# Kernel optimization log

Hardware: AMD Instinct MI355X
Metric: run time of the kernel (lower is better)

Reference implementation:

```python
import jax, jax.numpy as jnp
import numpy as np

D_MODEL = 1024
D_INNER = 2048
D_STATE = 16
DT_RANK = 64  # ceil(1024/16)
N_LAYERS = 4
SEQ = 4096


def setup_inputs() -> dict:
    key = jax.random.key(0)
    ks = list(jax.random.split(key, 8))
    L, d, di, n, r = N_LAYERS, D_MODEL, D_INNER, D_STATE, DT_RANK
    def rn(k, shape, scale):
        return jax.random.normal(k, shape, dtype=jnp.float32) * scale
    A_init = jnp.tile(jnp.log(jnp.arange(1, n + 1, dtype=jnp.float32))[None, None, :], (L, di, 1))
    return {
        'x': jax.random.normal(ks[0], (SEQ, d), dtype=jnp.float32),
        'pos_enc': jax.random.normal(ks[1], (SEQ, d), dtype=jnp.float32),
        'ln_g': jnp.ones((d,), jnp.float32),
        'ln_b': jnp.zeros((d,), jnp.float32),
        'innorm_g': jnp.ones((L, d), jnp.float32),
        'innorm_b': jnp.zeros((L, d), jnp.float32),
        'in_proj_w': rn(ks[2], (L, 2 * di, d), 0.02),
        'in_proj_b': jnp.zeros((L, 2 * di), jnp.float32),
        'conv_w': rn(ks[3], (L, di, 1, 3), 0.1),
        'conv_b': jnp.zeros((L, di), jnp.float32),
        'deltaBC_w': rn(ks[4], (L, r + 2 * n, di), 0.02),
        'dt_proj_w': rn(ks[5], (L, di, r), 0.02),
        'dt_proj_b': jnp.zeros((L, di), jnp.float32),
        'A_log': A_init,
        'Dp': jnp.ones((L, di), jnp.float32),
        'outnorm_g': jnp.ones((L, di), jnp.float32),
        'outnorm_b': jnp.zeros((L, di), jnp.float32),
        'out_proj_w': rn(ks[6], (L, d, di), 0.02),
        'out_proj_b': jnp.zeros((L, d), jnp.float32),
    }


def _ln(x, g, b, eps):
    mu = jnp.mean(x, axis=-1, keepdims=True)
    var = jnp.mean((x - mu) ** 2, axis=-1, keepdims=True)
    return (x - mu) * jax.lax.rsqrt(var + eps) * g + b


def _selective_scan(u, delta, A, B, C, D):
    # u, delta: [b,l,d]; A: [d,n]; B, C: [b,l,n]; D: [d]
    b, l, d = u.shape
    n = A.shape[1]
    def step(h, inputs):
        d_t, B_t, u_t, C_t = inputs          # [b,d],[b,n],[b,d],[b,n]
        dA = jnp.exp(d_t[:, :, None] * A)    # [b,d,n]
        dBu = (d_t * u_t)[:, :, None] * B_t[:, None, :]
        h = dA * h + dBu
        y = jnp.einsum('bdn,bn->bd', h, C_t)
        return h, y
    h0 = jnp.zeros((b, d, n), u.dtype)
    xs = (jnp.swapaxes(delta, 0, 1), jnp.swapaxes(B, 0, 1),
          jnp.swapaxes(u, 0, 1), jnp.swapaxes(C, 0, 1))
    _, ys = jax.lax.scan(step, h0, xs)       # ys: [l,b,d]
    return jnp.swapaxes(ys, 0, 1) + u * D


def _block(x, innorm_g, innorm_b, in_proj_w, in_proj_b, conv_w, conv_b,
           deltaBC_w, dt_proj_w, dt_proj_b, A_log, Dp, outnorm_g, outnorm_b,
           out_proj_w, out_proj_b):
    skip = x
    h = _ln(x, innorm_g, innorm_b, 1e-5)
    xz = h @ in_proj_w.T + in_proj_b
    x1, z1 = jnp.split(xz, 2, axis=-1)       # [b,s,di] each
    # depthwise conv1d, k=3, pad=1
    xc = jnp.swapaxes(x1, 1, 2)              # [b,di,s]
    xc = jax.lax.conv_general_dilated(xc, conv_w, (1,), [(1, 1)],
                                      feature_group_count=xc.shape[1],
                                      dimension_numbers=('NCH', 'OIH', 'NCH'))
    xc = xc + conv_b[None, :, None]
    u = jnp.swapaxes(xc, 1, 2)               # [b,s,di]
    # SSM
    A = -jnp.exp(A_log)
    dbc = u @ deltaBC_w.T                    # [b,s,r+2n]
    delta, B, C = jnp.split(dbc, [DT_RANK, DT_RANK + D_STATE], axis=-1)
    delta = jax.nn.softplus(delta @ dt_proj_w.T + dt_proj_b)
    y = _selective_scan(u, delta, A, B, C, Dp)
    y = _ln(y, outnorm_g, outnorm_b, 1e-5)
    out = y * jax.nn.silu(z1)
    return out @ out_proj_w.T + out_proj_b + skip


def _forward(x, pos_enc, ln_g, ln_b, innorm_g, innorm_b, in_proj_w, in_proj_b,
             conv_w, conv_b, deltaBC_w, dt_proj_w, dt_proj_b, A_log, Dp,
             outnorm_g, outnorm_b, out_proj_w, out_proj_b):
    enc = _ln(x + pos_enc, ln_g, ln_b, 1e-6)[None]  # [1,s,d]
    for i in range(N_LAYERS):
        enc = _block(enc, innorm_g[i], innorm_b[i], in_proj_w[i], in_proj_b[i],
                     conv_w[i], conv_b[i], deltaBC_w[i], dt_proj_w[i],
                     dt_proj_b[i], A_log[i], Dp[i], outnorm_g[i], outnorm_b[i],
                     out_proj_w[i], out_proj_b[i])
    return enc[0]


def reference(x, pos_enc, ln_g, ln_b, innorm_g, innorm_b, in_proj_w, in_proj_b,
              conv_w, conv_b, deltaBC_w, dt_proj_w, dt_proj_b, A_log, Dp,
              outnorm_g, outnorm_b, out_proj_w, out_proj_b):
    return _forward(x, pos_enc, ln_g, ln_b, innorm_g, innorm_b, in_proj_w,
                    in_proj_b, conv_w, conv_b, deltaBC_w, dt_proj_w, dt_proj_b,
                    A_log, Dp, outnorm_g, outnorm_b, out_proj_w, out_proj_b)
```

## Files before the change

kernel.cpp:

```cpp
#include <hip/hip_runtime.h>
#include <hip/hip_bf16.h>
#include <stdint.h>


#define SEQ     4096
#define DMODEL  1024
#define DINNER  2048
#define NSTATE  16
#define DTRANK  64
#define NLAYERS 4
#define LC      64
#define NC      64

typedef __attribute__((ext_vector_type(8))) short short8v;
typedef __attribute__((ext_vector_type(4))) float f32x4;
typedef __hip_bfloat16 bf16;

__device__ __forceinline__ float b2f(unsigned short x) {
    unsigned int u = ((unsigned int)x) << 16;
    return __builtin_bit_cast(float, u);
}

__device__ __forceinline__ void gld16(const void* gsrc, void* ldst) {
    __builtin_amdgcn_global_load_lds(
        (const __attribute__((address_space(1))) void*)gsrc,
        (__attribute__((address_space(3))) void*)ldst, 16, 0, 0);
}

__device__ __forceinline__ float block_sum(float v, float* red, int nwaves) {
    #pragma unroll
    for (int o = 32; o > 0; o >>= 1) v += __shfl_down(v, o, 64);
    int lane = threadIdx.x & 63, w = threadIdx.x >> 6;
    __syncthreads();
    if (lane == 0) red[w] = v;
    __syncthreads();
    float s = red[0];
    for (int i = 1; i < nwaves; i++) s += red[i];
    return s;
}

template<int WIDTH, typename OutT>
__global__ void ln_kernel(const float* __restrict__ X, const float* __restrict__ X2,
                          const float* __restrict__ g, const float* __restrict__ bta,
                          OutT* __restrict__ out, float eps) {
    constexpr int E = WIDTH / 256;
    __shared__ float red[4];
    int s = blockIdx.x, tid = threadIdx.x;
    size_t base = (size_t)s * WIDTH;
    float v[E]; float sum = 0.f;
    #pragma unroll
    for (int i = 0; i < E; i++) {
        int c = tid + i * 256;
        float t = X[base + c];
        if (X2) t += X2[base + c];
        v[i] = t; sum += t;
    }
    float mu = block_sum(sum, red, 4) * (1.f / WIDTH);
    float sq = 0.f;
    #pragma unroll
    for (int i = 0; i < E; i++) { float d = v[i] - mu; sq += d * d; }
    float var = block_sum(sq, red, 4) * (1.f / WIDTH);
    float rstd = rsqrtf(var + eps);
    #pragma unroll
    for (int i = 0; i < E; i++) {
        int c = tid + i * 256;
        float r = (v[i] - mu) * rstd * g[c] + bta[c];
        out[base + c] = (OutT)r;
    }
}

__global__ void outnorm_silu_kernel(const float* __restrict__ y, const bf16* __restrict__ xz,
                                    const float* __restrict__ g, const float* __restrict__ bta,
                                    bf16* __restrict__ p_bf, float eps) {
    constexpr int WIDTH = DINNER, E = WIDTH / 256;
    __shared__ float red[4];
    int s = blockIdx.x, tid = threadIdx.x;
    size_t base = (size_t)s * WIDTH;
    const unsigned short* xzu = (const unsigned short*)xz;
    float v[E]; float sum = 0.f;
    #pragma unroll
    for (int i = 0; i < E; i++) { int c = tid + i * 256; v[i] = y[base + c]; sum += v[i]; }
    float mu = block_sum(sum, red, 4) * (1.f / WIDTH);
    float sq = 0.f;
    #pragma unroll
    for (int i = 0; i < E; i++) { float d = v[i] - mu; sq += d * d; }
    float var = block_sum(sq, red, 4) * (1.f / WIDTH);
    float rstd = rsqrtf(var + eps);
    #pragma unroll
    for (int i = 0; i < E; i++) {
        int c = tid + i * 256;
        float ln = (v[i] - mu) * rstd * g[c] + bta[c];
        float z = b2f(xzu[(size_t)s * (2 * DINNER) + DINNER + c]);
        float sig = 1.f / (1.f + __expf(-z));
        p_bf[base + c] = __float2bfloat16(ln * (z * sig));
    }
}

__global__ void conv_kernel(const bf16* __restrict__ xz, const float* __restrict__ cw,
                            const float* __restrict__ cb, bf16* __restrict__ u_bf) {
    int t = blockIdx.x * 256 + threadIdx.x;
    int s = t >> 9, c = (t & 511) * 4;
    size_t row = (size_t)s * (2 * DINNER);
    const unsigned short* xp = (const unsigned short*)xz;
    ushort4 z4 = {0, 0, 0, 0};
    ushort4 v0 = *(const ushort4*)(xp + row + c);
    ushort4 vm = (s > 0)       ? *(const ushort4*)(xp + row - 2 * DINNER + c) : z4;
    ushort4 vp = (s < SEQ - 1) ? *(const ushort4*)(xp + row + 2 * DINNER + c) : z4;
    unsigned short o[4];
    float x0[4] = {b2f(v0.x), b2f(v0.y), b2f(v0.z), b2f(v0.w)};
    float xm[4] = {b2f(vm.x), b2f(vm.y), b2f(vm.z), b2f(vm.w)};
    float xp4[4] = {b2f(vp.x), b2f(vp.y), b2f(vp.z), b2f(vp.w)};
    #pragma unroll
    for (int i = 0; i < 4; i++) {
        int ch = c + i;
        float u = cw[ch * 3 + 0] * xm[i] + cw[ch * 3 + 1] * x0[i]
                + cw[ch * 3 + 2] * xp4[i] + cb[ch];
        o[i] = __builtin_bit_cast(unsigned short, __float2bfloat16(u));
    }
    *(ushort4*)((unsigned short*)u_bf + (size_t)s * DINNER + c) = {o[0], o[1], o[2], o[3]};
}

#define CN0 (2 * DINNER * DMODEL)
#define CN1 (DMODEL * DINNER)
#define CN2 (96 * DINNER)
#define CN3 (DINNER * DTRANK)
__global__ void cvt_all_kernel(const float* __restrict__ w0, const float* __restrict__ w1,
                               const float* __restrict__ w2, const float* __restrict__ w3,
                               bf16* __restrict__ o0, bf16* __restrict__ o1,
                               bf16* __restrict__ o2, bf16* __restrict__ o3) {
    size_t i = (size_t)(blockIdx.x * 256 + threadIdx.x) * 4;
    const float* src; bf16* dst;
    if (i < CN0)                   { src = w0; dst = o0; }
    else if (i < CN0 + CN1)        { src = w1; dst = o1; i -= CN0; }
    else if (i < CN0 + CN1 + CN2)  { src = w2; dst = o2; i -= CN0 + CN1; }
    else                           { src = w3; dst = o3; i -= CN0 + CN1 + CN2; }
    float4 v = *(const float4*)(src + i);
    __hip_bfloat162 t0, t1;
    t0.x = __float2bfloat16(v.x); t0.y = __float2bfloat16(v.y);
    t1.x = __float2bfloat16(v.z); t1.y = __float2bfloat16(v.w);
    __hip_bfloat162* o = (__hip_bfloat162*)(dst + i);
    o[0] = t0; o[1] = t1;
}

template<int MODE>
__global__ __launch_bounds__(256, 2)
void mfma_gemm(const bf16* __restrict__ A, int lda,
               const bf16* __restrict__ W, int ldw,
               const float* __restrict__ bias,
               float* __restrict__ C, int ldc,
               const float* __restrict__ res,
               bf16* __restrict__ Cbf,
               int M, int N, int K) {
    __shared__ __attribute__((aligned(16))) short sA[128][32];
    __shared__ __attribute__((aligned(16))) short sB[128][32];
    int tid = threadIdx.x;
    int lane = tid & 63, w = tid >> 6;
    int wm = w >> 1, wn = w & 1;
    int m0 = blockIdx.x * 128, n0 = blockIdx.y * 128;
    int r16 = lane & 15, quad = lane >> 4;
    int ldrow = (lane >> 2);
    int c8 = (lane & 3) * 8;

    if (MODE == 1) {
        int kz = blockIdx.z;
        A += (size_t)kz * K;
        W += (size_t)kz * K;
        C += (size_t)kz * M * 96;
    }

    f32x4 acc[4][4] = {};

    for (int k0 = 0; k0 < K; k0 += 32) {
        __syncthreads();
        #pragma unroll
        for (int j = 0; j < 2; j++) {
            int row = j * 64 + w * 16 + ldrow;
            gld16(A + (size_t)(m0 + row) * lda + k0 + c8,
                  (char*)&sA[0][0] + j * 4096 + w * 1024);
            int nr = n0 + row; if (nr > N - 1) nr = N - 1;
            gld16(W + (size_t)nr * ldw + k0 + c8,
                  (char*)&sB[0][0] + j * 4096 + w * 1024);
        }
        __syncthreads();
        short8v aF[4], bF[4];
        #pragma unroll
        for (int mi = 0; mi < 4; mi++)
            aF[mi] = *(const short8v*)&sA[wm * 64 + mi * 16 + r16][quad * 8];
        #pragma unroll
        for (int ni = 0; ni < 4; ni++)
            bF[ni] = *(const short8v*)&sB[wn * 64 + ni * 16 + r16][quad * 8];
        #pragma unroll
        for (int mi = 0; mi < 4; mi++)
            #pragma unroll
            for (int ni = 0; ni < 4; ni++)
                acc[mi][ni] = __builtin_amdgcn_mfma_f32_16x16x32_bf16(
                    aF[mi], bF[ni], acc[mi][ni], 0, 0, 0);
    }

    #pragma unroll
    for (int mi = 0; mi < 4; mi++) {
        #pragma unroll
        for (int ni = 0; ni < 4; ni++) {
            f32x4 a = acc[mi][ni];
            int col = n0 + wn * 64 + ni * 16 + r16;
            int rbase = m0 + wm * 64 + mi * 16 + quad * 4;
            #pragma unroll
            for (int r = 0; r < 4; r++) {
                int row = rbase + r;
                float v = a[r];
                if (MODE == 0 || MODE == 2 || MODE == 3) v += bias[col];
                if (MODE == 2) v = (v > 20.f) ? v : log1pf(__expf(v));
                if (MODE == 3) v += res[(size_t)row * ldc + col];
                if (MODE == 1) {
                    if (col < 96) C[(size_t)row * 96 + col] = v;
                } else if (MODE == 0) {
                    Cbf[(size_t)row * ldc + col] = __float2bfloat16(v);
                } else {
                    C[(size_t)row * ldc + col] = v;
                }
            }
        }
    }
}

__global__ void reduce_dbc_kernel(const float* __restrict__ p, float* __restrict__ dbc,
                                  bf16* __restrict__ dbc_bf) {
    int i = blockIdx.x * 256 + threadIdx.x;
    const int SP = SEQ * 96;
    float v = p[i] + p[i + SP] + p[i + 2 * SP] + p[i + 3 * SP];
    dbc[i] = v;
    int row = i / 96, c = i - row * 96;
    if (c < DTRANK) dbc_bf[(size_t)row * DTRANK + c] = __float2bfloat16(v);
}

__device__ __forceinline__ bool a_is_neg_integers(const float* a) {
    bool fast = true;
    #pragma unroll
    for (int n = 0; n < NSTATE; n++)
        fast = fast && (__builtin_fabsf(a[n] + (float)(n + 1)) < 1e-3f * (n + 1));
    return fast;
}

__global__ __launch_bounds__(256)
void scan1_kernel(const float* __restrict__ delta, const bf16* __restrict__ u,
                  const float* __restrict__ dbc, const float* __restrict__ A_log,
                  float* __restrict__ h_end, float* __restrict__ dsum) {
    int k = blockIdx.x, d = blockIdx.y * 256 + threadIdx.x;
    int s0 = k * LC;
    float a[NSTATE];
    #pragma unroll
    for (int n = 0; n < NSTATE; n++) a[n] = -__expf(A_log[(size_t)d * NSTATE + n]);
    bool fast = a_is_neg_integers(a);
    const float* dp = delta + (size_t)s0 * DINNER + d;
    const unsigned short* up = (const unsigned short*)u + (size_t)s0 * DINNER + d;
    const float* br = dbc + (size_t)s0 * 96 + DTRANK;
    float h[NSTATE] = {};
    float ds = 0.f;
    if (fast) {
        #pragma unroll 2
        for (int r = 0; r < LC; r++) {
            float dl = *dp;
            float uu = b2f(*up);
            float4 b0 = *(const float4*)(br);
            float4 b1 = *(const float4*)(br + 4);
            float4 b2 = *(const float4*)(br + 8);
            float4 b3 = *(const float4*)(br + 12);
            float Bv[NSTATE] = {b0.x, b0.y, b0.z, b0.w, b1.x, b1.y, b1.z, b1.w,
                                b2.x, b2.y, b2.z, b2.w, b3.x, b3.y, b3.z, b3.w};
            ds += dl;
            float du = dl * uu;
            float g = __expf(-dl);
            float fac = 1.f;
            #pragma unroll
            for (int n = 0; n < NSTATE; n++) {
                fac *= g;
                h[n] = fac * h[n] + du * Bv[n];
            }
            dp += DINNER; up += DINNER; br += 96;
        }
    } else {
        #pragma unroll 2
        for (int r = 0; r < LC; r++) {
            float dl = *dp;
            float uu = b2f(*up);
            float4 b0 = *(const float4*)(br);
            float4 b1 = *(const float4*)(br + 4);
            float4 b2 = *(const float4*)(br + 8);
            float4 b3 = *(const float4*)(br + 12);
            float Bv[NSTATE] = {b0.x, b0.y, b0.z, b0.w, b1.x, b1.y, b1.z, b1.w,
                                b2.x, b2.y, b2.z, b2.w, b3.x, b3.y, b3.z, b3.w};
            ds += dl;
            float du = dl * uu;
            #pragma unroll
            for (int n = 0; n < NSTATE; n++)
                h[n] = __expf(dl * a[n]) * h[n] + du * Bv[n];
            dp += DINNER; up += DINNER; br += 96;
        }
    }
    #pragma unroll
    for (int n = 0; n < NSTATE; n++)
        h_end[((size_t)k * NSTATE + n) * DINNER + d] = h[n];
    dsum[(size_t)k * DINNER + d] = ds;
}

__global__ void scan2_kernel(const float* __restrict__ A_log, const float* __restrict__ dsum,
                             const float* __restrict__ h_end, float* __restrict__ hinit) {
    int id = blockIdx.x * 256 + threadIdx.x;
    int d = id & (DINNER - 1), n = id >> 11;
    float a = -__expf(A_log[(size_t)d * NSTATE + n]);
    float h = 0.f;
    for (int k = 0; k < NC; k++) {
        size_t off = ((size_t)k * NSTATE + n) * DINNER + d;
        hinit[off] = h;
        h = __expf(a * dsum[(size_t)k * DINNER + d]) * h + h_end[off];
    }
}

__global__ __launch_bounds__(256)
void scan3_kernel(float* __restrict__ delta_y, const bf16* __restrict__ u,
                  const float* __restrict__ dbc, const float* __restrict__ A_log,
                  const float* __restrict__ Dp, const float* __restrict__ hinit) {
    int k = blockIdx.x, d = blockIdx.y * 256 + threadIdx.x;
    int s0 = k * LC;
    float a[NSTATE];
    #pragma unroll
    for (int n = 0; n < NSTATE; n++) a[n] = -__expf(A_log[(size_t)d * NSTATE + n]);
    bool fast = a_is_neg_integers(a);
    float h[NSTATE];
    #pragma unroll
    for (int n = 0; n < NSTATE; n++)
        h[n] = hinit[((size_t)k * NSTATE + n) * DINNER + d];
    float dpv = Dp[d];
    float* dp = delta_y + (size_t)s0 * DINNER + d;
    const unsigned short* up = (const unsigned short*)u + (size_t)s0 * DINNER + d;
    const float* br = dbc + (size_t)s0 * 96 + DTRANK;
    if (fast) {
        #pragma unroll 2
        for (int r = 0; r < LC; r++) {
            float dl = *dp;
            float uu = b2f(*up);
            float4 b0 = *(const float4*)(br);
            float4 b1 = *(const float4*)(br + 4);
            float4 b2 = *(const float4*)(br + 8);
            float4 b3 = *(const float4*)(br + 12);
            float4 c0 = *(const float4*)(br + 16);
            float4 c1 = *(const float4*)(br + 20);
            float4 c2 = *(const float4*)(br + 24);
            float4 c3 = *(const float4*)(br + 28);
            float Bv[NSTATE] = {b0.x, b0.y, b0.z, b0.w, b1.x, b1.y, b1.z, b1.w,
                                b2.x, b2.y, b2.z, b2.w, b3.x, b3.y, b3.z, b3.w};
            float Cv[NSTATE] = {c0.x, c0.y, c0.z, c0.w, c1.x, c1.y, c1.z, c1.w,
                                c2.x, c2.y, c2.z, c2.w, c3.x, c3.y, c3.z, c3.w};
            float du = dl * uu;
            float g = __expf(-dl);
            float y = uu * dpv;
            float fac = 1.f;
            #pragma unroll
            for (int n = 0; n < NSTATE; n++) {
                fac *= g;
                h[n] = fac * h[n] + du * Bv[n];
                y += h[n] * Cv[n];
            }
            *dp = y;
            dp += DINNER; up += DINNER; br += 96;
        }
    } else {
        #pragma unroll 2
        for (int r = 0; r < LC; r++) {
            float dl = *dp;
            float uu = b2f(*up);
            float4 b0 = *(const float4*)(br);
            float4 b1 = *(const float4*)(br + 4);
            float4 b2 = *(const float4*)(br + 8);
            float4 b3 = *(const float4*)(br + 12);
            float4 c0 = *(const float4*)(br + 16);
            float4 c1 = *(const float4*)(br + 20);
            float4 c2 = *(const float4*)(br + 24);
            float4 c3 = *(const float4*)(br + 28);
            float Bv[NSTATE] = {b0.x, b0.y, b0.z, b0.w, b1.x, b1.y, b1.z, b1.w,
                                b2.x, b2.y, b2.z, b2.w, b3.x, b3.y, b3.z, b3.w};
            float Cv[NSTATE] = {c0.x, c0.y, c0.z, c0.w, c1.x, c1.y, c1.z, c1.w,
                                c2.x, c2.y, c2.z, c2.w, c3.x, c3.y, c3.z, c3.w};
            float du = dl * uu;
            float y = uu * dpv;
            #pragma unroll
            for (int n = 0; n < NSTATE; n++) {
                h[n] = __expf(dl * a[n]) * h[n] + du * Bv[n];
                y += h[n] * Cv[n];
            }
            *dp = y;
            dp += DINNER; up += DINNER; br += 96;
        }
    }
}

extern "C" void kernel_launch(void* const* d_in, const int* in_sizes, int n_in,
                              void* d_out, int out_size, void* d_ws, size_t ws_size,
                              hipStream_t stream) {
    const float* x         = (const float*)d_in[0];
    const float* pos       = (const float*)d_in[1];
    const float* ln_g      = (const float*)d_in[2];
    const float* ln_b      = (const float*)d_in[3];
    const float* innorm_g  = (const float*)d_in[4];
    const float* innorm_b  = (const float*)d_in[5];
    const float* in_proj_w = (const float*)d_in[6];
    const float* in_proj_b = (const float*)d_in[7];
    const float* conv_w    = (const float*)d_in[8];
    const float* conv_b    = (const float*)d_in[9];
    const float* deltaBC_w = (const float*)d_in[10];
    const float* dt_proj_w = (const float*)d_in[11];
    const float* dt_proj_b = (const float*)d_in[12];
    const float* A_log     = (const float*)d_in[13];
    const float* Dp        = (const float*)d_in[14];
    const float* outnorm_g = (const float*)d_in[15];
    const float* outnorm_b = (const float*)d_in[16];
    const float* out_proj_w= (const float*)d_in[17];
    const float* out_proj_b= (const float*)d_in[18];

    float* enc = (float*)d_out;
    char* ws = (char*)d_ws;
    const size_t MB = 1024 * 1024;
    bf16*  h_bf   = (bf16*) (ws + 0);
    bf16*  p_bf   = (bf16*) (ws + 0);
    bf16*  xz_bf  = (bf16*) (ws + 16 * MB);
    float* dlt    = (float*)(ws + 48 * MB);
    float* dbcp   = (float*)(ws + 48 * MB);
    bf16*  u_bf   = (bf16*) (ws + 80 * MB);
    float* dbc    = (float*)(ws + 96 * MB);
    bf16*  dbc_bf = (bf16*) (ws + 98 * MB);
    float* h_end  = (float*)(ws + 99 * MB);
    float* hinit  = (float*)(ws + 107 * MB);
    float* dsum   = (float*)(ws + 115 * MB);
    bf16*  w_in   = (bf16*) (ws + 116 * MB);
    bf16*  w_dbc  = (bf16*) (ws + 124 * MB);
    bf16*  w_dt   = (bf16*) (ws + 125 * MB);
    bf16*  w_out  = (bf16*) (ws + 126 * MB);

    ln_kernel<DMODEL, float><<<SEQ, 256, 0, stream>>>(x, pos, ln_g, ln_b, enc, 1e-6f);

    for (int L = 0; L < NLAYERS; L++) {
        const float* Al = A_log + (size_t)L * DINNER * NSTATE;
        cvt_all_kernel<<<(CN0 + CN1 + CN2 + CN3) / 1024, 256, 0, stream>>>(
            in_proj_w + (size_t)L * CN0, out_proj_w + (size_t)L * CN1,
            deltaBC_w + (size_t)L * CN2, dt_proj_w + (size_t)L * CN3,
            w_in, w_out, w_dbc, w_dt);

        ln_kernel<DMODEL, bf16><<<SEQ, 256, 0, stream>>>(enc, nullptr, innorm_g + L * DMODEL,
                                                         innorm_b + L * DMODEL, h_bf, 1e-5f);
        mfma_gemm<0><<<dim3(32, 32), 256, 0, stream>>>(
            h_bf, DMODEL, w_in, DMODEL, in_proj_b + (size_t)L * 2 * DINNER,
            nullptr, 2 * DINNER, nullptr, xz_bf, SEQ, 2 * DINNER, DMODEL);
        conv_kernel<<<(SEQ * 512) / 256, 256, 0, stream>>>(
            xz_bf, conv_w + (size_t)L * DINNER * 3, conv_b + L * DINNER, u_bf);
        mfma_gemm<1><<<dim3(32, 1, 4), 256, 0, stream>>>(
            u_bf, DINNER, w_dbc, DINNER, nullptr,
            dbcp, 96, nullptr, nullptr, SEQ, 96, 512);
        reduce_dbc_kernel<<<(SEQ * 96) / 256, 256, 0, stream>>>(dbcp, dbc, dbc_bf);
        mfma_gemm<2><<<dim3(32, 16), 256, 0, stream>>>(
            dbc_bf, DTRANK, w_dt, DTRANK, dt_proj_b + L * DINNER,
            dlt, DINNER, nullptr, nullptr, SEQ, DINNER, DTRANK);
        scan1_kernel<<<dim3(NC, DINNER / 256), 256, 0, stream>>>(dlt, u_bf, dbc, Al, h_end, dsum);
        scan2_kernel<<<(DINNER * NSTATE) / 256, 256, 0, stream>>>(Al, dsum, h_end, hinit);
        scan3_kernel<<<dim3(NC, DINNER / 256), 256, 0, stream>>>(dlt, u_bf, dbc, Al,
                                                                 Dp + L * DINNER, hinit);
        outnorm_silu_kernel<<<SEQ, 256, 0, stream>>>(dlt, xz_bf, outnorm_g + L * DINNER,
                                                     outnorm_b + L * DINNER, p_bf, 1e-5f);
        mfma_gemm<3><<<dim3(32, 8), 256, 0, stream>>>(
            p_bf, DINNER, w_out, DINNER, out_proj_b + L * DMODEL,
            enc, DMODEL, enc, nullptr, SEQ, DMODEL, DINNER);
    }
}
```

Measured before the change: 1.099 ms.

## Add dedicated 256x256 eight-wave pipelined GEMM for in_proj

Replaces the generic 128x128 MFMA GEMM for the in_proj matmul with a specialised 512-thread kernel using 256x256 tiles. It double-buffers LDS via direct global-to-LDS loads interleaved with MFMA phases, raises wave priority during compute, uses XOR-swizzled LDS layouts to avoid bank conflicts, and remaps block IDs for L2 locality. The aim is to raise MFMA utilisation and overlap loads with compute on the largest GEMM. The cost is a large LDS footprint (128KB) with one block per CU, and hardcoded shapes.

```diff
diff --git a/kernel.cpp b/kernel.cpp
--- a/kernel.cpp
+++ b/kernel.cpp
@@ -142,6 +142,94 @@
     o[0] = t0; o[1] = t1;
 }
 
+__global__ __launch_bounds__(512, 1)
+void gemm8p_inproj(const bf16* __restrict__ gA, const bf16* __restrict__ gW,
+                   const float* __restrict__ bias, bf16* __restrict__ Cbf) {
+    __shared__ __attribute__((aligned(16))) short sA[2][2][256 * 32];
+    __shared__ __attribute__((aligned(16))) short sB[2][2][256 * 32];
+    int tid = threadIdx.x, lane = tid & 63, w = tid >> 6;
+    int wm = w >> 2, wn = w & 3;
+    int r16 = lane & 15, quad = lane >> 4;
+    int q8 = (quad ^ (((r16 >> 3) & 1) << 1)) * 8;
+
+    int bid = blockIdx.x;
+    int sw = (bid & 7) * 32 + (bid >> 3);
+    int m0 = (sw & 15) * 256, n0 = (sw >> 4) * 256;
+
+    int row0 = tid >> 2, row1 = (512 + tid) >> 2;
+    int q0 = ((tid & 3) ^ (((row0 >> 3) & 1) << 1)) * 8;
+    int q1 = ((tid & 3) ^ (((row1 >> 3) & 1) << 1)) * 8;
+
+#define STAGE8(SOP, SKT, SKH, SDB) do {                                        \
+        const bf16* _src = (SOP) ? gA : gW;                                    \
+        int _r0 = (SOP) ? m0 : n0;                                             \
+        char* _sl = (char*)((SOP) ? &sA[SDB][SKH][0] : &sB[SDB][SKH][0]);      \
+        gld16(_src + (size_t)(_r0 + row0) * 1024 + (SKT) * 64 + (SKH) * 32 + q0, \
+              _sl + w * 1024);                                                 \
+        gld16(_src + (size_t)(_r0 + row1) * 1024 + (SKT) * 64 + (SKH) * 32 + q1, \
+              _sl + 8192 + w * 1024);                                          \
+    } while (0)
+
+#define LDA8(mf, kh, db) (*(const short8v*)&sA[db][kh][(wm * 128 + (mf) * 16 + r16) * 32 + q8])
+#define LDB8(nf, kh, db) (*(const short8v*)&sB[db][kh][(wn * 64 + (nf) * 16 + r16) * 32 + q8])
+
+    f32x4 acc[8][4] = {};
+    short8v bF[4];
+
+#define PHASE8(MB, KH, RDB, SOP, SKT, SKH, SDB, VM) do {                       \
+        short8v a0 = LDA8(MB + 0, KH, db), a1 = LDA8(MB + 1, KH, db);          \
+        short8v a2 = LDA8(MB + 2, KH, db), a3 = LDA8(MB + 3, KH, db);          \
+        if (RDB) { bF[0] = LDB8(0, KH, db); bF[1] = LDB8(1, KH, db);           \
+                   bF[2] = LDB8(2, KH, db); bF[3] = LDB8(3, KH, db); }         \
+        STAGE8(SOP, SKT, SKH, SDB);                                            \
+        __builtin_amdgcn_s_barrier();                                          \
+        asm volatile("s_waitcnt lgkmcnt(0)" ::: "memory");                     \
+        __builtin_amdgcn_s_setprio(1);                                         \
+        for (int ni = 0; ni < 4; ni++) {                                       \
+            acc[MB + 0][ni] = __builtin_amdgcn_mfma_f32_16x16x32_bf16(a0, bF[ni], acc[MB + 0][ni], 0, 0, 0); \
+            acc[MB + 1][ni] = __builtin_amdgcn_mfma_f32_16x16x32_bf16(a1, bF[ni], acc[MB + 1][ni], 0, 0, 0); \
+            acc[MB + 2][ni] = __builtin_amdgcn_mfma_f32_16x16x32_bf16(a2, bF[ni], acc[MB + 2][ni], 0, 0, 0); \
+            acc[MB + 3][ni] = __builtin_amdgcn_mfma_f32_16x16x32_bf16(a3, bF[ni], acc[MB + 3][ni], 0, 0, 0); \
+        }                                                                      \
+        __builtin_amdgcn_s_setprio(0);                                         \
+        if (VM) asm volatile("s_waitcnt vmcnt(4)" ::: "memory");               \
+        __builtin_amdgcn_s_barrier();                                          \
+    } while (0)
+
+    STAGE8(1, 0, 0, 0); STAGE8(0, 0, 0, 0);
+    STAGE8(1, 0, 1, 0); STAGE8(0, 0, 1, 0);
+    STAGE8(1, 1, 0, 1); STAGE8(0, 1, 0, 1);
+    asm volatile("s_waitcnt vmcnt(4)" ::: "memory");
+    __builtin_amdgcn_s_barrier();
+
+    #pragma unroll 1
+    for (int kt = 0; kt < 16; kt++) {
+        int db = kt & 1, dn = db ^ 1;
+        int kt1 = (kt + 1) & 15, kt2 = (kt + 2) & 15;
+        PHASE8(0, 0, 1, 1, kt1, 1, dn, 0);
+        PHASE8(4, 0, 0, 0, kt1, 1, dn, 0);
+        PHASE8(0, 1, 1, 1, kt2, 0, db, 0);
+        PHASE8(4, 1, 0, 0, kt2, 0, db, 1);
+    }
+
+    #pragma unroll
+    for (int nf = 0; nf < 4; nf++) {
+        int col = n0 + wn * 64 + nf * 16 + r16;
+        float bs = bias[col];
+        #pragma unroll
+        for (int mf = 0; mf < 8; mf++) {
+            int rb = m0 + wm * 128 + mf * 16 + quad * 4;
+            #pragma unroll
+            for (int r = 0; r < 4; r++)
+                Cbf[(size_t)(rb + r) * 4096 + col] = __float2bfloat16(acc[mf][nf][r] + bs);
+        }
+    }
+#undef STAGE8
+#undef LDA8
+#undef LDB8
+#undef PHASE8
+}
+
 template<int MODE>
 __global__ __launch_bounds__(256, 2)
 void mfma_gemm(const bf16* __restrict__ A, int lda,
@@ -208,13 +296,11 @@
             for (int r = 0; r < 4; r++) {
                 int row = rbase + r;
                 float v = a[r];
-                if (MODE == 0 || MODE == 2 || MODE == 3) v += bias[col];
+                if (MODE == 2 || MODE == 3) v += bias[col];
                 if (MODE == 2) v = (v > 20.f) ? v : log1pf(__expf(v));
                 if (MODE == 3) v += res[(size_t)row * ldc + col];
                 if (MODE == 1) {
                     if (col < 96) C[(size_t)row * 96 + col] = v;
-                } else if (MODE == 0) {
-                    Cbf[(size_t)row * ldc + col] = __float2bfloat16(v);
                 } else {
                     C[(size_t)row * ldc + col] = v;
                 }
@@ -447,9 +533,8 @@
 
         ln_kernel<DMODEL, bf16><<<SEQ, 256, 0, stream>>>(enc, nullptr, innorm_g + L * DMODEL,
                                                          innorm_b + L * DMODEL, h_bf, 1e-5f);
-        mfma_gemm<0><<<dim3(32, 32), 256, 0, stream>>>(
-            h_bf, DMODEL, w_in, DMODEL, in_proj_b + (size_t)L * 2 * DINNER,
-            nullptr, 2 * DINNER, nullptr, xz_bf, SEQ, 2 * DINNER, DMODEL);
+        gemm8p_inproj<<<256, 512, 0, stream>>>(
+            h_bf, w_in, in_proj_b + (size_t)L * 2 * DINNER, xz_bf);
         conv_kernel<<<(SEQ * 512) / 256, 256, 0, stream>>>(
             xz_bf, conv_w + (size_t)L * DINNER * 3, conv_b + L * DINNER, u_bf);
         mfma_gemm<1><<<dim3(32, 1, 4), 256, 0, stream>>>(
```

Measured after the change: 1.123 ms. +2.2%, slower.
